# Performance work log

Hardware: AMD Instinct MI355X
Metric: run time of the kernel (lower is better)

## Reference

```python
import jax, jax.numpy as jnp
import numpy as np

POOL = 3            # pool_size for this detection level
CENTER_TOP_NUM = 100
CENTER_THRES = 0.1
INST_THRES = 0.4


def _pool2d(x, op, k):
    """Stride-1 SAME pooling on NCHW, matching torch pad=(k-1)//2.
    avg matches torch avg_pool2d default count_include_pad=True (divide by k*k)."""
    if op == 'max':
        return jax.lax.reduce_window(x, -jnp.inf, jax.lax.max,
                                     (1, 1, k, k), (1, 1, 1, 1), 'SAME')
    s = jax.lax.reduce_window(x, 0.0, jax.lax.add,
                              (1, 1, k, k), (1, 1, 1, 1), 'SAME')
    return s / (k * k)


def setup_inputs() -> dict:
    key = jax.random.key(0)
    k1, k2, k3 = jax.random.split(key, 3)
    return {
        'thing_map':    jax.random.normal(k1, (1, 80, 128, 256), jnp.float32),
        'kernel_space': jax.random.normal(k2, (1, 256, 128, 256), jnp.float32),
        'embeddings':   jax.random.normal(k3, (1, 256, 256, 512), jnp.float32),
    }


def reference(thing_map, kernel_space, embeddings):
    B, C, H, W = thing_map.shape
    # --- peak detection (CenterNet-style) ---
    centers = jax.nn.sigmoid(thing_map)
    centers = (centers + _pool2d(centers, 'avg', POOL)) * 0.5
    fmap_max = _pool2d(centers, 'max', 3)
    peak_mask = (fmap_max == centers).astype(centers.dtype)
    centers = centers * peak_mask
    # --- topk over (class, h, w) ---
    K = min(H * W, CENTER_TOP_NUM // 2)  # 50
    flat = centers.reshape(B, C * H * W)
    scores, idx = jax.lax.top_k(flat, K)          # [B, K], sorted descending
    cats = idx // (H * W)                          # [B, K] class ids
    spatial = idx % (H * W)                        # [B, K] spatial index
    # masked_select(score > thres) replaced by a static-shape validity mask
    valid = (scores > CENTER_THRES).astype(scores.dtype)
    # --- sample kernels at peak locations ---
    D = kernel_space.shape[1]
    kflat = kernel_space.reshape(B, D, H * W)      # batch dims (h w)
    kernels = jnp.take_along_axis(kflat, spatial[:, None, :], axis=2)  # [B, D, K]
    kernels = kernels.transpose(0, 2, 1)           # [B, K, D]
    # --- maskifier: dynamic conv of kernels over embeddings, then sigmoid ---
    thing_masks = jax.nn.sigmoid(
        jnp.einsum('bkd,bdhw->bkhw', kernels, embeddings))  # [B, K, He, We]
    # --- mask-based score rescoring ---
    binm = (thing_masks > INST_THRES).astype(thing_masks.dtype)
    score_factor = (thing_masks * binm).sum((-2, -1))
    score_factor = score_factor / jnp.maximum(binm.sum((-2, -1)), 1e-8)
    scores = scores * score_factor * valid
    return thing_masks, scores, cats
```

## Files before the change

### kernel.cpp

```cpp
#include <hip/hip_runtime.h>
#include <hip/hip_bf16.h>
#include <math.h>


constexpr int C   = 80;
constexpr int H   = 128;
constexpr int W   = 256;
constexpr int HW  = H * W;
constexpr int CHW = C * HW;
constexpr int D   = 256;
constexpr int NPIX = 256 * 512;
constexpr int K   = 50;
constexpr int KP  = 52;
constexpr int NBINS = 4096;
constexpr int MAXCAND = 8192;
constexpr int SEL_CAP = 4096;
constexpr int MASK_ELEMS = K * NPIX;

constexpr int OFF_CENTERS = 0;
constexpr int OFF_HIST    = CHW;
constexpr int OFF_CUTBIN  = OFF_HIST + NBINS;
constexpr int OFF_CCOUNT  = OFF_CUTBIN + 1;
constexpr int OFF_CVAL    = OFF_CCOUNT + 1;
constexpr int OFF_CIDX    = OFF_CVAL + MAXCAND;
constexpr int OFF_TSCORE  = OFF_CIDX + MAXCAND;
constexpr int OFF_TSPAT   = OFF_TSCORE + K;
constexpr int OFF_TCAT    = OFF_TSPAT + K;
constexpr int OFF_A       = OFF_TCAT + K;
constexpr int OFF_FNUM    = OFF_A + KP * D;
constexpr int OFF_FDEN    = OFF_FNUM + K;
constexpr int OFF_PEAKV   = OFF_FDEN + K;

#define REP13(X) X(0) X(1) X(2) X(3) X(4) X(5) X(6) X(7) X(8) X(9) X(10) X(11) X(12)

__device__ __forceinline__ float sigmoidf(float x) {
    return 1.0f / (1.0f + expf(-x));
}

__global__ void centers_kernel(const float* __restrict__ x, float* __restrict__ ws) {
    if (blockIdx.x == 0) {
        int* wsi = (int*)ws;
        for (int i = threadIdx.x; i < NBINS; i += 256) wsi[OFF_HIST + i] = 0;
        if (threadIdx.x < K) { ws[OFF_FNUM + threadIdx.x] = 0.0f; ws[OFF_FDEN + threadIdx.x] = 0.0f; }
        if (threadIdx.x == 0) wsi[OFF_CCOUNT] = 0;
    }
    int idx = blockIdx.x * 256 + threadIdx.x;
    if (idx >= CHW) return;
    int w = idx & (W - 1);
    int h = (idx >> 8) & (H - 1);
    int cbase = idx & ~(HW - 1);
    float s0 = sigmoidf(x[idx]);
    float sum = 0.0f;
    #pragma unroll
    for (int dh = -1; dh <= 1; dh++) {
        int hh = h + dh;
        if ((unsigned)hh >= (unsigned)H) continue;
        #pragma unroll
        for (int dw = -1; dw <= 1; dw++) {
            int ww = w + dw;
            if ((unsigned)ww >= (unsigned)W) continue;
            sum += sigmoidf(x[cbase + (hh << 8) + ww]);
        }
    }
    ws[OFF_CENTERS + idx] = 0.5f * (s0 + sum / 9.0f);
}

__device__ __forceinline__ float peak_value(const float* cen, int idx) {
    int w = idx & (W - 1);
    int h = (idx >> 8) & (H - 1);
    int cbase = idx & ~(HW - 1);
    float c0 = cen[idx];
    float m = c0;
    #pragma unroll
    for (int dh = -1; dh <= 1; dh++) {
        int hh = h + dh;
        if ((unsigned)hh >= (unsigned)H) continue;
        #pragma unroll
        for (int dw = -1; dw <= 1; dw++) {
            int ww = w + dw;
            if ((unsigned)ww >= (unsigned)W) continue;
            m = fmaxf(m, cen[cbase + (hh << 8) + ww]);
        }
    }
    return (c0 == m) ? c0 : -1.0f;
}

__device__ __forceinline__ int value_bin(float v) {
    int b = (int)(v * (float)NBINS);
    return b > NBINS - 1 ? NBINS - 1 : b;
}

__global__ void hist_kernel(float* ws, float* peakv) {
    int idx = blockIdx.x * 256 + threadIdx.x;
    if (idx >= CHW) return;
    const float* cen = ws + OFF_CENTERS;
    float v = peak_value(cen, idx);
    if (peakv) peakv[idx] = v;
    if (v >= 0.0f) {
        atomicAdd((int*)ws + OFF_HIST + value_bin(v), 1);
    }
}

__global__ void scan_kernel(float* ws) {
    __shared__ int chunk[256];
    const int* hist = (const int*)ws + OFF_HIST;
    int t = threadIdx.x;
    int s = 0;
    #pragma unroll
    for (int b = t * 16; b < t * 16 + 16; b++) s += hist[b];
    chunk[t] = s;
    __syncthreads();
    if (t == 0) {
        int cum = 0, cutbin = 0;
        bool found = false;
        for (int ch = 255; ch >= 0 && !found; ch--) {
            if (cum + chunk[ch] >= K) {
                for (int b = ch * 16 + 15; b >= ch * 16; b--) {
                    cum += hist[b];
                    if (cum >= K) { cutbin = b; found = true; break; }
                }
            } else {
                cum += chunk[ch];
            }
        }
        ((int*)ws)[OFF_CUTBIN] = found ? cutbin : 0;
    }
}

__global__ void gather_kernel(float* ws, const float* peakv) {
    int idx = blockIdx.x * 256 + threadIdx.x;
    if (idx >= CHW) return;
    float v = peakv ? peakv[idx] : peak_value(ws + OFF_CENTERS, idx);
    if (v >= 0.0f) {
        int cutbin = ((const int*)ws)[OFF_CUTBIN];
        if (value_bin(v) >= cutbin) {
            int pos = atomicAdd((int*)ws + OFF_CCOUNT, 1);
            if (pos < MAXCAND) {
                ws[OFF_CVAL + pos] = v;
                ((int*)ws)[OFF_CIDX + pos] = idx;
            }
        }
    }
}

__global__ void select_kernel(float* ws) {
    __shared__ float sv[SEL_CAP];
    __shared__ int   si[SEL_CAP];
    __shared__ unsigned smask[MAXCAND / 32];
    const float* cval = ws + OFF_CVAL;
    const int*   cidx = (const int*)ws + OFF_CIDX;
    int n = ((const int*)ws)[OFF_CCOUNT];
    if (n > MAXCAND) n = MAXCAND;
    int t = threadIdx.x;

    int cap = n < SEL_CAP ? n : SEL_CAP;
    for (int q = t; q < cap; q += 64) { sv[q] = cval[q]; si[q] = cidx[q]; }
    for (int q = t; q < MAXCAND / 32; q += 64) smask[q] = 0u;
    __syncthreads();

    for (int j = 0; j < K; j++) {
        float bv = -1e30f; int bi = 0x7fffffff; int bp = -1;
        for (int q = t; q < n; q += 64) {
            if (smask[q >> 5] & (1u << (q & 31))) continue;
            float v; int id;
            if (q < SEL_CAP) { v = sv[q]; id = si[q]; }
            else             { v = cval[q]; id = cidx[q]; }
            if (v > bv || (v == bv && id < bi)) { bv = v; bi = id; bp = q; }
        }
        #pragma unroll
        for (int m = 1; m < 64; m <<= 1) {
            float ov = __shfl_xor(bv, m);
            int   oi = __shfl_xor(bi, m);
            int   op = __shfl_xor(bp, m);
            if (ov > bv || (ov == bv && oi < bi)) { bv = ov; bi = oi; bp = op; }
        }
        if (t == 0) {
            float score = (bp >= 0) ? bv : 0.0f;
            int   idx   = (bp >= 0) ? bi : 0;
            ws[OFF_TSCORE + j] = score;
            ((int*)ws)[OFF_TSPAT + j] = idx & (HW - 1);
            ((int*)ws)[OFF_TCAT + j]  = idx >> 15;
            if (bp >= 0) smask[bp >> 5] |= (1u << (bp & 31));
        }
        __syncthreads();
    }
}

__global__ void gatherA_kernel(const float* __restrict__ ksp, float* __restrict__ ws) {
    int k = blockIdx.x;
    int d = threadIdx.x;
    float v = 0.0f;
    if (k < K) {
        int sp = ((const int*)ws)[OFF_TSPAT + k];
        v = ksp[d * HW + sp];
    }
    ws[OFF_A + d * KP + k] = v;
}

#define FMAROW(i) { const float4 a_ = Arow[i]; \
    c##i.x = fmaf(e, a_.x, c##i.x); \
    c##i.y = fmaf(e, a_.y, c##i.y); \
    c##i.z = fmaf(e, a_.z, c##i.z); \
    c##i.w = fmaf(e, a_.w, c##i.w); }

__global__ __launch_bounds__(256) void gemm_kernel(
        const float* __restrict__ emb,
        const float* __restrict__ At,
        float* __restrict__ out) {
    const int n = blockIdx.x * 256 + threadIdx.x;
    const float4* __restrict__ Af = (const float4*)At;

#define DECLC(i) float4 c##i = make_float4(0.0f, 0.0f, 0.0f, 0.0f);
    REP13(DECLC)
#undef DECLC

    const float* __restrict__ ep = emb + n;
    float cur0 = ep[(size_t)0 * NPIX];
    float cur1 = ep[(size_t)1 * NPIX];
    float cur2 = ep[(size_t)2 * NPIX];
    float cur3 = ep[(size_t)3 * NPIX];

    for (int d = 0; d < D - 4; d += 4) {
        const float* q = ep + (size_t)(d + 4) * NPIX;
        float nxt0 = q[0];
        float nxt1 = q[(size_t)1 * NPIX];
        float nxt2 = q[(size_t)2 * NPIX];
        float nxt3 = q[(size_t)3 * NPIX];
        { const float4* Arow = Af + (d + 0) * 13; const float e = cur0; REP13(FMAROW) }
        { const float4* Arow = Af + (d + 1) * 13; const float e = cur1; REP13(FMAROW) }
        { const float4* Arow = Af + (d + 2) * 13; const float e = cur2; REP13(FMAROW) }
        { const float4* Arow = Af + (d + 3) * 13; const float e = cur3; REP13(FMAROW) }
        cur0 = nxt0; cur1 = nxt1; cur2 = nxt2; cur3 = nxt3;
    }
    { const float4* Arow = Af + (D - 4) * 13; const float e = cur0; REP13(FMAROW) }
    { const float4* Arow = Af + (D - 3) * 13; const float e = cur1; REP13(FMAROW) }
    { const float4* Arow = Af + (D - 2) * 13; const float e = cur2; REP13(FMAROW) }
    { const float4* Arow = Af + (D - 1) * 13; const float e = cur3; REP13(FMAROW) }

    float* op = out + n;
#define EPI(i) \
    if (4*(i)+0 < K) op[(size_t)(4*(i)+0) * NPIX] = 1.0f/(1.0f+expf(-c##i.x)); \
    if (4*(i)+1 < K) op[(size_t)(4*(i)+1) * NPIX] = 1.0f/(1.0f+expf(-c##i.y)); \
    if (4*(i)+2 < K) op[(size_t)(4*(i)+2) * NPIX] = 1.0f/(1.0f+expf(-c##i.z)); \
    if (4*(i)+3 < K) op[(size_t)(4*(i)+3) * NPIX] = 1.0f/(1.0f+expf(-c##i.w));
    REP13(EPI)
#undef EPI
}

__global__ __launch_bounds__(256) void rescore_kernel(
        const float* __restrict__ masks,
        float* __restrict__ fnum,
        float* __restrict__ fden) {
    const int k = blockIdx.x;
    const float4* mk = (const float4*)(masks + (size_t)k * NPIX);
    float a = 0.0f; float b = 0.0f;
    int base = blockIdx.y * 2048 + threadIdx.x;
    #pragma unroll
    for (int r = 0; r < 8; r++) {
        float4 v = mk[base + r * 256];
        if (v.x > 0.4f) { a += v.x; b += 1.0f; }
        if (v.y > 0.4f) { a += v.y; b += 1.0f; }
        if (v.z > 0.4f) { a += v.z; b += 1.0f; }
        if (v.w > 0.4f) { a += v.w; b += 1.0f; }
    }
    a += __shfl_xor(a, 1);  b += __shfl_xor(b, 1);
    a += __shfl_xor(a, 2);  b += __shfl_xor(b, 2);
    a += __shfl_xor(a, 4);  b += __shfl_xor(b, 4);
    a += __shfl_xor(a, 8);  b += __shfl_xor(b, 8);
    a += __shfl_xor(a, 16); b += __shfl_xor(b, 16);
    a += __shfl_xor(a, 32); b += __shfl_xor(b, 32);
    __shared__ float sa[4], sb[4];
    int wave = threadIdx.x >> 6;
    if ((threadIdx.x & 63) == 0) { sa[wave] = a; sb[wave] = b; }
    __syncthreads();
    if (threadIdx.x == 0) {
        atomicAdd(&fnum[k], sa[0] + sa[1] + sa[2] + sa[3]);
        atomicAdd(&fden[k], sb[0] + sb[1] + sb[2] + sb[3]);
    }
}

__global__ void finalize_kernel(const float* __restrict__ ws, float* __restrict__ out) {
    int j = threadIdx.x;
    if (j < K) {
        float s = ws[OFF_TSCORE + j];
        float num = ws[OFF_FNUM + j];
        float den = ws[OFF_FDEN + j];
        float factor = num / fmaxf(den, 1e-8f);
        float valid = (s > 0.1f) ? 1.0f : 0.0f;
        out[MASK_ELEMS + j]     = s * factor * valid;
        out[MASK_ELEMS + K + j] = (float)(((const int*)ws)[OFF_TCAT + j]);
    }
}

extern "C" void kernel_launch(void* const* d_in, const int* in_sizes, int n_in,
                              void* d_out, int out_size, void* d_ws, size_t ws_size,
                              hipStream_t stream) {
    const float* thing_map = (const float*)d_in[0];
    const float* ksp       = (const float*)d_in[1];
    const float* emb       = (const float*)d_in[2];
    float* out = (float*)d_out;
    float* ws  = (float*)d_ws;

    bool have_peakv = ws_size >= (size_t)(OFF_PEAKV + CHW) * sizeof(float);
    float* peakv = have_peakv ? (ws + OFF_PEAKV) : nullptr;

    centers_kernel<<<CHW / 256, 256, 0, stream>>>(thing_map, ws);
    hist_kernel<<<CHW / 256, 256, 0, stream>>>(ws, peakv);
    scan_kernel<<<1, 256, 0, stream>>>(ws);
    gather_kernel<<<CHW / 256, 256, 0, stream>>>(ws, peakv);
    select_kernel<<<1, 64, 0, stream>>>(ws);
    gatherA_kernel<<<KP, D, 0, stream>>>(ksp, ws);
    gemm_kernel<<<NPIX / 256, 256, 0, stream>>>(emb, ws + OFF_A, out);
    rescore_kernel<<<dim3(K, 16), 256, 0, stream>>>(out, ws + OFF_FNUM, ws + OFF_FDEN);
    finalize_kernel<<<1, 64, 0, stream>>>(ws, out);
}
```

Baseline: 442.2 us.

## Fuse sigmoid/avg-pool/peak detection into one tiled kernel with compacted peak list

Replaces the separate centers and histogram kernels with one shared-memory tiled kernel. It computes the sigmoid, the average-pool centers and the 3x3 max-pool peak test per 64x4 tile and builds a block-local histogram before flushing it to global memory. Peaks are stream-compacted into a global list using wave ballots, so the gather kernel only scans peaks instead of every element, and workspace zeroing moves to a memset. This removes the full-size centers and peak-value round trips through global memory and cuts global atomics, at the cost of halo recomputation, a 16KB shared histogram per block that limits occupancy, and a fixed peak-list cap of CHW/4.

```diff
diff --git a/kernel.cpp b/kernel.cpp
--- a/kernel.cpp
+++ b/kernel.cpp
@@ -17,72 +17,29 @@
 constexpr int SEL_CAP = 4096;
 constexpr int MASK_ELEMS = K * NPIX;
 
-constexpr int OFF_CENTERS = 0;
-constexpr int OFF_HIST    = CHW;
-constexpr int OFF_CUTBIN  = OFF_HIST + NBINS;
-constexpr int OFF_CCOUNT  = OFF_CUTBIN + 1;
-constexpr int OFF_CVAL    = OFF_CCOUNT + 1;
-constexpr int OFF_CIDX    = OFF_CVAL + MAXCAND;
-constexpr int OFF_TSCORE  = OFF_CIDX + MAXCAND;
-constexpr int OFF_TSPAT   = OFF_TSCORE + K;
-constexpr int OFF_TCAT    = OFF_TSPAT + K;
-constexpr int OFF_A       = OFF_TCAT + K;
-constexpr int OFF_FNUM    = OFF_A + KP * D;
-constexpr int OFF_FDEN    = OFF_FNUM + K;
-constexpr int OFF_PEAKV   = OFF_FDEN + K;
+constexpr int CAP = CHW / 4;
+
+constexpr int OFF_PKVAL  = 0;
+constexpr int OFF_PKIDX  = CAP;
+constexpr int OFF_HIST   = 2 * CAP;
+constexpr int OFF_CUTBIN = OFF_HIST + NBINS;
+constexpr int OFF_PCOUNT = OFF_CUTBIN + 1;
+constexpr int OFF_CCOUNT = OFF_PCOUNT + 1;
+constexpr int OFF_FNUM   = OFF_CCOUNT + 1;
+constexpr int OFF_FDEN   = OFF_FNUM + K;
+constexpr int OFF_CVAL   = OFF_FDEN + K;
+constexpr int OFF_CIDX   = OFF_CVAL + MAXCAND;
+constexpr int OFF_TSCORE = OFF_CIDX + MAXCAND;
+constexpr int OFF_TSPAT  = OFF_TSCORE + K;
+constexpr int OFF_TCAT   = OFF_TSPAT + K;
+constexpr int OFF_A      = (OFF_TCAT + K + 3) & ~3;
+constexpr int WS_END     = OFF_A + KP * D;
+constexpr int ZERO_WORDS = NBINS + 3 + 2 * K;
 
 #define REP13(X) X(0) X(1) X(2) X(3) X(4) X(5) X(6) X(7) X(8) X(9) X(10) X(11) X(12)
 
 __device__ __forceinline__ float sigmoidf(float x) {
     return 1.0f / (1.0f + expf(-x));
-}
-
-__global__ void centers_kernel(const float* __restrict__ x, float* __restrict__ ws) {
-    if (blockIdx.x == 0) {
-        int* wsi = (int*)ws;
-        for (int i = threadIdx.x; i < NBINS; i += 256) wsi[OFF_HIST + i] = 0;
-        if (threadIdx.x < K) { ws[OFF_FNUM + threadIdx.x] = 0.0f; ws[OFF_FDEN + threadIdx.x] = 0.0f; }
-        if (threadIdx.x == 0) wsi[OFF_CCOUNT] = 0;
-    }
-    int idx = blockIdx.x * 256 + threadIdx.x;
-    if (idx >= CHW) return;
-    int w = idx & (W - 1);
-    int h = (idx >> 8) & (H - 1);
-    int cbase = idx & ~(HW - 1);
-    float s0 = sigmoidf(x[idx]);
-    float sum = 0.0f;
-    #pragma unroll
-    for (int dh = -1; dh <= 1; dh++) {
-        int hh = h + dh;
-        if ((unsigned)hh >= (unsigned)H) continue;
-        #pragma unroll
-        for (int dw = -1; dw <= 1; dw++) {
-            int ww = w + dw;
-            if ((unsigned)ww >= (unsigned)W) continue;
-            sum += sigmoidf(x[cbase + (hh << 8) + ww]);
-        }
-    }
-    ws[OFF_CENTERS + idx] = 0.5f * (s0 + sum / 9.0f);
-}
-
-__device__ __forceinline__ float peak_value(const float* cen, int idx) {
-    int w = idx & (W - 1);
-    int h = (idx >> 8) & (H - 1);
-    int cbase = idx & ~(HW - 1);
-    float c0 = cen[idx];
-    float m = c0;
-    #pragma unroll
-    for (int dh = -1; dh <= 1; dh++) {
-        int hh = h + dh;
-        if ((unsigned)hh >= (unsigned)H) continue;
-        #pragma unroll
-        for (int dw = -1; dw <= 1; dw++) {
-            int ww = w + dw;
-            if ((unsigned)ww >= (unsigned)W) continue;
-            m = fmaxf(m, cen[cbase + (hh << 8) + ww]);
-        }
-    }
-    return (c0 == m) ? c0 : -1.0f;
 }
 
 __device__ __forceinline__ int value_bin(float v) {
@@ -90,14 +47,91 @@
     return b > NBINS - 1 ? NBINS - 1 : b;
 }
 
-__global__ void hist_kernel(float* ws, float* peakv) {
-    int idx = blockIdx.x * 256 + threadIdx.x;
-    if (idx >= CHW) return;
-    const float* cen = ws + OFF_CENTERS;
-    float v = peak_value(cen, idx);
-    if (peakv) peakv[idx] = v;
-    if (v >= 0.0f) {
-        atomicAdd((int*)ws + OFF_HIST + value_bin(v), 1);
+constexpr int TW = 64, TH = 4;
+constexpr int SW = TW + 4, SH = TH + 4;
+constexpr int CW = TW + 2, CH2 = TH + 2;
+
+__global__ __launch_bounds__(256) void peaks_kernel(
+        const float* __restrict__ x, float* __restrict__ ws) {
+    __shared__ float ssig[SH][SW];
+    __shared__ float scen[CH2][CW];
+    __shared__ int   shist[NBINS];
+    __shared__ int   wcnt[4];
+    __shared__ int   bbase;
+
+    const int tid = threadIdx.x;
+    for (int i = tid; i < NBINS; i += 256) shist[i] = 0;
+
+    const int b  = blockIdx.x;
+    const int c  = b >> 7;
+    const int t  = b & 127;
+    const int h0 = (t >> 2) * TH;
+    const int w0 = (t & 3) * TW;
+    const float* xc = x + c * HW;
+
+    for (int l = tid; l < SH * SW; l += 256) {
+        int r = l / SW, q = l - r * SW;
+        int h = h0 + r - 2, w = w0 + q - 2;
+        float s = 0.0f;
+        if ((unsigned)h < (unsigned)H && (unsigned)w < (unsigned)W)
+            s = sigmoidf(xc[(h << 8) + w]);
+        ssig[r][q] = s;
+    }
+    __syncthreads();
+
+    for (int l = tid; l < CH2 * CW; l += 256) {
+        int r = l / CW, q = l - r * CW;
+        int h = h0 + r - 1, w = w0 + q - 1;
+        float cv = -INFINITY;
+        if ((unsigned)h < (unsigned)H && (unsigned)w < (unsigned)W) {
+            float s0 = ssig[r + 1][q + 1];
+            float sum = 0.0f;
+            #pragma unroll
+            for (int dh = 0; dh < 3; dh++)
+                #pragma unroll
+                for (int dw = 0; dw < 3; dw++)
+                    sum += ssig[r + dh][q + dw];
+            cv = 0.5f * (s0 + sum / 9.0f);
+        }
+        scen[r][q] = cv;
+    }
+    __syncthreads();
+
+    const int dw = tid & 63, dh = tid >> 6;
+    float c0 = scen[dh + 1][dw + 1];
+    float m = c0;
+    #pragma unroll
+    for (int i = 0; i < 3; i++)
+        #pragma unroll
+        for (int j = 0; j < 3; j++)
+            m = fmaxf(m, scen[dh + i][dw + j]);
+    const bool peak = (c0 == m);
+    const int idx = c * HW + ((h0 + dh) << 8) + (w0 + dw);
+
+    if (peak) atomicAdd(&shist[value_bin(c0)], 1);
+
+    unsigned long long mk = __ballot(peak);
+    const int lane = tid & 63, wv = tid >> 6;
+    if (lane == 0) wcnt[wv] = __popcll(mk);
+    __syncthreads();
+    if (tid == 0) {
+        int e0 = wcnt[0], e1 = wcnt[1], e2 = wcnt[2], e3 = wcnt[3];
+        wcnt[0] = 0; wcnt[1] = e0; wcnt[2] = e0 + e1; wcnt[3] = e0 + e1 + e2;
+        bbase = atomicAdd((int*)ws + OFF_PCOUNT, e0 + e1 + e2 + e3);
+    }
+    __syncthreads();
+    if (peak) {
+        int pos = bbase + wcnt[wv] + __popcll(mk & ((1ull << lane) - 1ull));
+        if (pos < CAP) {
+            ws[OFF_PKVAL + pos] = c0;
+            ((int*)ws)[OFF_PKIDX + pos] = idx;
+        }
+    }
+
+    __syncthreads();
+    for (int i = tid; i < NBINS; i += 256) {
+        int v = shist[i];
+        if (v) atomicAdd((int*)ws + OFF_HIST + i, v);
     }
 }
 
@@ -127,18 +161,18 @@
     }
 }
 
-__global__ void gather_kernel(float* ws, const float* peakv) {
-    int idx = blockIdx.x * 256 + threadIdx.x;
-    if (idx >= CHW) return;
-    float v = peakv ? peakv[idx] : peak_value(ws + OFF_CENTERS, idx);
-    if (v >= 0.0f) {
-        int cutbin = ((const int*)ws)[OFF_CUTBIN];
-        if (value_bin(v) >= cutbin) {
-            int pos = atomicAdd((int*)ws + OFF_CCOUNT, 1);
-            if (pos < MAXCAND) {
-                ws[OFF_CVAL + pos] = v;
-                ((int*)ws)[OFF_CIDX + pos] = idx;
-            }
+__global__ void gather_kernel(float* ws) {
+    int q = blockIdx.x * 256 + threadIdx.x;
+    int n = ((const int*)ws)[OFF_PCOUNT];
+    if (n > CAP) n = CAP;
+    if (q >= n) return;
+    float v = ws[OFF_PKVAL + q];
+    int cutbin = ((const int*)ws)[OFF_CUTBIN];
+    if (value_bin(v) >= cutbin) {
+        int pos = atomicAdd((int*)ws + OFF_CCOUNT, 1);
+        if (pos < MAXCAND) {
+            ws[OFF_CVAL + pos] = v;
+            ((int*)ws)[OFF_CIDX + pos] = ((const int*)ws)[OFF_PKIDX + q];
         }
     }
 }
@@ -301,13 +335,11 @@
     float* out = (float*)d_out;
     float* ws  = (float*)d_ws;
 
-    bool have_peakv = ws_size >= (size_t)(OFF_PEAKV + CHW) * sizeof(float);
-    float* peakv = have_peakv ? (ws + OFF_PEAKV) : nullptr;
-
-    centers_kernel<<<CHW / 256, 256, 0, stream>>>(thing_map, ws);
-    hist_kernel<<<CHW / 256, 256, 0, stream>>>(ws, peakv);
+    hipMemsetAsync(ws + OFF_HIST, 0, (size_t)ZERO_WORDS * 4, stream);
+
+    peaks_kernel<<<C * 128, 256, 0, stream>>>(thing_map, ws);
     scan_kernel<<<1, 256, 0, stream>>>(ws);
-    gather_kernel<<<CHW / 256, 256, 0, stream>>>(ws, peakv);
+    gather_kernel<<<CAP / 256, 256, 0, stream>>>(ws);
     select_kernel<<<1, 64, 0, stream>>>(ws);
     gatherA_kernel<<<KP, D, 0, stream>>>(ksp, ws);
     gemm_kernel<<<NPIX / 256, 256, 0, stream>>>(emb, ws + OFF_A, out);
```

Measured after the change: 446.3 us. No clear change (+0.9%).
